# Performance work log

Measured on AMD Instinct MI355X. Metric: run time of the kernel, lower is better.

The kernel has to match this reference:

```python
import jax, jax.numpy as jnp
import numpy as np

T = 200000  # stack depth
V = 130     # vocab_size == input_dim
H = 512     # hid_dim
L = 2       # n_layers


def setup_inputs() -> dict:
    key = jax.random.key(0)
    ks = jax.random.split(key, 24)
    s = 0.05
    inp = {
        "input": jax.random.normal(ks[0], (1, 1, V), jnp.float32),
        "prev_Val": jax.random.normal(ks[1], (T, V), jnp.float32),
        "prev_stg": jax.random.uniform(ks[2], (T,), jnp.float32),
        "prev_read": jax.random.normal(ks[3], (V,), jnp.float32),
        "prev_h": jax.random.normal(ks[4], (L, 1, H), jnp.float32) * 0.1,
        "prev_c": jax.random.normal(ks[5], (L, 1, H), jnp.float32) * 0.1,
        # LSTM layer 0 (pytorch layout: W_ih (4H, in), W_hh (4H, H), gates i,f,g,o)
        "W_ih0": jax.random.normal(ks[6], (4 * H, V), jnp.float32) * s,
        "W_hh0": jax.random.normal(ks[7], (4 * H, H), jnp.float32) * s,
        "b_ih0": jax.random.normal(ks[8], (4 * H,), jnp.float32) * s,
        "b_hh0": jax.random.normal(ks[9], (4 * H,), jnp.float32) * s,
        # LSTM layer 1
        "W_ih1": jax.random.normal(ks[10], (4 * H, H), jnp.float32) * s,
        "W_hh1": jax.random.normal(ks[11], (4 * H, H), jnp.float32) * s,
        "b_ih1": jax.random.normal(ks[12], (4 * H,), jnp.float32) * s,
        "b_hh1": jax.random.normal(ks[13], (4 * H,), jnp.float32) * s,
        # gate heads (original inits these to zeros; random here to exercise math)
        "Wd": jax.random.normal(ks[14], (H,), jnp.float32) * s,
        "Bd": jax.random.normal(ks[15], (), jnp.float32) * s,
        "Wu": jax.random.normal(ks[16], (H,), jnp.float32) * s,
        "Bu": jax.random.normal(ks[17], (), jnp.float32) * s,
        "Wv": jax.random.normal(ks[18], (H, V), jnp.float32) * s,
        "Bv": jax.random.normal(ks[19], (V,), jnp.float32) * s,
        "Wo": jax.random.normal(ks[20], (H, H), jnp.float32) * s,
        "Bo": jax.random.normal(ks[21], (H,), jnp.float32) * s,
    }
    return inp


def _lstm_cell(x, h, c, Wih, Whh, bih, bhh):
    # x: (1, in), h/c: (1, H)
    g = x @ Wih.T + h @ Whh.T + bih + bhh  # (1, 4H)
    i, f, gg, o = jnp.split(g, 4, axis=-1)
    c2 = jax.nn.sigmoid(f) * c + jax.nn.sigmoid(i) * jnp.tanh(gg)
    h2 = jax.nn.sigmoid(o) * jnp.tanh(c2)
    return h2, c2


def reference(input, prev_Val, prev_stg, prev_read, prev_h, prev_c,
              W_ih0, W_hh0, b_ih0, b_hh0, W_ih1, W_hh1, b_ih1, b_hh1,
              Wd, Bd, Wu, Bu, Wv, Bv, Wo, Bo):
    x = (input + prev_read)[0]  # (1, V), seq_len == 1, batch == 1
    h1, c1 = _lstm_cell(x, prev_h[0], prev_c[0], W_ih0, W_hh0, b_ih0, b_hh0)
    h2, c2 = _lstm_cell(h1, prev_h[1], prev_c[1], W_ih1, W_hh1, b_ih1, b_hh1)
    output = h2  # (1, H)

    dt = jax.nn.sigmoid(output @ Wd + Bd)[0]      # scalar push strength
    ut = jax.nn.sigmoid(output @ Wu + Bu)[0]      # scalar pop strength
    vt = jnp.tanh(output @ Wv + Bv)               # (1, V) pushed value
    ot = jnp.tanh(output @ Wo + Bo)               # (1, H) controller output

    Val = jnp.concatenate([prev_Val, vt], axis=0)  # (T+1, V)

    # pop pass (top -> bottom): stg[i] = max(0, prev_stg[i] - max(0, ut)); ut -= stg[i]
    def pop_step(u, s):
        sn = jnp.maximum(0.0, s - jnp.maximum(0.0, u))
        return u - sn, sn
    _, stg_popped = jax.lax.scan(pop_step, ut, prev_stg, reverse=True)
    stg = jnp.concatenate([stg_popped, dt[None]])  # (T+1,)

    # read pass (top -> bottom): coef = min(stg[i], max(0, read)); read -= stg[i]
    def read_step(r, s):
        coef = jnp.minimum(s, jnp.maximum(0.0, r))
        return r - s, coef
    _, coefs = jax.lax.scan(read_step, jnp.asarray(1.0, stg.dtype), stg, reverse=True)
    rt = coefs @ Val  # (V,)

    h_new = jnp.stack([h1, h2])  # (L, 1, H)
    c_new = jnp.stack([c1, c2])
    return ot, Val, stg, rt, h_new, c_new
```

## Files before the change

kernel.cpp:

```cpp
#include <hip/hip_runtime.h>

#define T_DEPTH 200000
#define V_DIM   130
#define H_DIM   512

#define OT_OFF   0
#define VAL_OFF  512
#define STG_OFF  26000642
#define RT_OFF   26200643
#define HN_OFF   26200773
#define CN_OFF   26201797

#define WS_G0     0
#define WS_H1     2048
#define WS_C1     2560
#define WS_G1     3072
#define WS_H2     5120
#define WS_C2     5632
#define WS_VTACC  6144
#define WS_OTACC  6274
#define WS_DTUT   6786
#define WS_VT     6788
#define WS_TOTAL  6918

static __device__ __forceinline__ float sigmoidf(float x) {
    return 1.0f / (1.0f + expf(-x));
}

__global__ void k_bulk(const float4* __restrict__ val_in,
                       const float2* __restrict__ stg_in,
                       float* __restrict__ out) {
    const int NV4 = (T_DEPTH * V_DIM) / 4;
    const int NS2 = T_DEPTH / 2;
    const int NT  = NV4 + NS2;
    float4* __restrict__ val_out = reinterpret_cast<float4*>(out + VAL_OFF);
    float2* __restrict__ stg_out = reinterpret_cast<float2*>(out + STG_OFF);
    int stride = gridDim.x * blockDim.x;
    for (int u = blockIdx.x * blockDim.x + threadIdx.x; u < NT; u += stride) {
        if (u < NV4) {
            val_out[u] = val_in[u];
        } else {
            int s = u - NV4;
            stg_out[s] = stg_in[s];
        }
    }
}

__global__ void k_g0(const float* __restrict__ Wih, const float* __restrict__ Whh,
                     const float* __restrict__ bih, const float* __restrict__ bhh,
                     const float* __restrict__ inp, const float* __restrict__ prd,
                     const float* __restrict__ h0, float* __restrict__ g) {
    int wave = threadIdx.x >> 6, lane = threadIdx.x & 63;
    int row = blockIdx.x * 4 + wave;
    const float* wr = Wih + row * V_DIM;
    const float* wh = Whh + row * H_DIM;
    float p = 0.f;
    for (int c = lane; c < V_DIM; c += 64) p += wr[c] * (inp[c] + prd[c]);
    for (int k = lane; k < H_DIM; k += 64) p += wh[k] * h0[k];
    for (int off = 32; off; off >>= 1) p += __shfl_down(p, off, 64);
    if (lane == 0) g[row] = p + bih[row] + bhh[row];
}

__global__ void k_g1(const float* __restrict__ Wih, const float* __restrict__ Whh,
                     const float* __restrict__ bih, const float* __restrict__ bhh,
                     const float* __restrict__ h1, const float* __restrict__ hprev,
                     float* __restrict__ g) {
    int wave = threadIdx.x >> 6, lane = threadIdx.x & 63;
    int row = blockIdx.x * 4 + wave;
    const float* wr = Wih + row * H_DIM;
    const float* wh = Whh + row * H_DIM;
    float p = 0.f;
    for (int k = lane; k < H_DIM; k += 64) p += wr[k] * h1[k] + wh[k] * hprev[k];
    for (int off = 32; off; off >>= 1) p += __shfl_down(p, off, 64);
    if (lane == 0) g[row] = p + bih[row] + bhh[row];
}

__global__ void k_cell(const float* __restrict__ g, const float* __restrict__ cprev,
                       float* __restrict__ h, float* __restrict__ c,
                       float* __restrict__ h_out, float* __restrict__ c_out) {
    int j = threadIdx.x;
    float ig = sigmoidf(g[j]);
    float fg = sigmoidf(g[H_DIM + j]);
    float gg = tanhf(g[2 * H_DIM + j]);
    float og = sigmoidf(g[3 * H_DIM + j]);
    float cn = fg * cprev[j] + ig * gg;
    float hn = og * tanhf(cn);
    h[j] = hn; c[j] = cn;
    h_out[j] = hn;
    c_out[j] = cn;
}

__global__ void k_heads(const float* __restrict__ h2, const float* __restrict__ Wv,
                        const float* __restrict__ Wo, float* __restrict__ vt_acc,
                        float* __restrict__ ot_acc) {
    int t = threadIdx.x;
    int b = blockIdx.x;
    float a0 = 0.f, a1 = 0.f, av = 0.f;
    for (int kk = 0; kk < 16; ++kk) {
        int k = b * 16 + kk;
        float hv = h2[k];
        a0 += hv * Wo[k * H_DIM + t];
        a1 += hv * Wo[k * H_DIM + t + 256];
        if (t < V_DIM) av += hv * Wv[k * V_DIM + t];
    }
    atomicAdd(&ot_acc[t], a0);
    atomicAdd(&ot_acc[t + 256], a1);
    if (t < V_DIM) atomicAdd(&vt_acc[t], av);
}

__global__ void k_hfin(const float* __restrict__ h2,
                       const float* __restrict__ Wd, const float* __restrict__ Bd,
                       const float* __restrict__ Wu, const float* __restrict__ Bu,
                       const float* __restrict__ Bv, const float* __restrict__ Bo,
                       const float* __restrict__ vt_acc, const float* __restrict__ ot_acc,
                       float* __restrict__ dtut, float* __restrict__ vt,
                       float* __restrict__ out) {
    __shared__ float sd[H_DIM], su[H_DIM];
    int t = threadIdx.x;
    sd[t] = h2[t] * Wd[t];
    su[t] = h2[t] * Wu[t];
    __syncthreads();
    for (int s = 256; s; s >>= 1) {
        if (t < s) { sd[t] += sd[t + s]; su[t] += su[t + s]; }
        __syncthreads();
    }
    if (t == 0) {
        float dt = sigmoidf(sd[0] + Bd[0]);
        float ut = sigmoidf(su[0] + Bu[0]);
        dtut[0] = dt; dtut[1] = ut;
        out[STG_OFF + T_DEPTH] = dt;
    }
    float ot = tanhf(ot_acc[t] + Bo[t]);
    out[OT_OFF + t] = ot;
    if (t < V_DIM) {
        float v = tanhf(vt_acc[t] + Bv[t]);
        vt[t] = v;
        out[VAL_OFF + T_DEPTH * V_DIM + t] = v;
    }
}

__global__ void k_top(const float* __restrict__ prev_stg, const float* __restrict__ prev_val,
                      const float* __restrict__ dtut, const float* __restrict__ vt,
                      float* __restrict__ out) {
    int t = threadIdx.x;
    float dt = dtut[0];
    float u  = dtut[1];
    float r  = 1.0f;
    float acc = 0.f;
    {
        float coef = fminf(dt, fmaxf(0.f, r));
        if (t < V_DIM) acc += coef * vt[t];
        r -= dt;
    }
    for (int i = T_DEPTH - 1; i >= 0; --i) {
        bool pop_active = (u > 0.f);
        if (!pop_active && r <= 0.f) break;
        float s  = prev_stg[i];
        float sn = fmaxf(0.f, s - fmaxf(0.f, u));
        u -= sn;
        if (pop_active && t == 0) out[STG_OFF + i] = sn;
        float coef = fminf(sn, fmaxf(0.f, r));
        r -= sn;
        if (coef > 0.f && t < V_DIM) acc += coef * prev_val[i * V_DIM + t];
    }
    if (t < V_DIM) out[RT_OFF + t] = acc;
}

extern "C" void kernel_launch(void* const* d_in, const int* in_sizes, int n_in,
                              void* d_out, int out_size, void* d_ws, size_t ws_size,
                              hipStream_t stream) {
    (void)in_sizes; (void)n_in; (void)out_size; (void)ws_size;
    const float* input     = (const float*)d_in[0];
    const float* prev_Val  = (const float*)d_in[1];
    const float* prev_stg  = (const float*)d_in[2];
    const float* prev_read = (const float*)d_in[3];
    const float* prev_h    = (const float*)d_in[4];
    const float* prev_c    = (const float*)d_in[5];
    const float* W_ih0 = (const float*)d_in[6];
    const float* W_hh0 = (const float*)d_in[7];
    const float* b_ih0 = (const float*)d_in[8];
    const float* b_hh0 = (const float*)d_in[9];
    const float* W_ih1 = (const float*)d_in[10];
    const float* W_hh1 = (const float*)d_in[11];
    const float* b_ih1 = (const float*)d_in[12];
    const float* b_hh1 = (const float*)d_in[13];
    const float* Wd = (const float*)d_in[14];
    const float* Bd = (const float*)d_in[15];
    const float* Wu = (const float*)d_in[16];
    const float* Bu = (const float*)d_in[17];
    const float* Wv = (const float*)d_in[18];
    const float* Bv = (const float*)d_in[19];
    const float* Wo = (const float*)d_in[20];
    const float* Bo = (const float*)d_in[21];

    float* out = (float*)d_out;
    float* ws  = (float*)d_ws;

    hipMemsetAsync(d_ws, 0, WS_TOTAL * sizeof(float), stream);

    k_bulk<<<4096, 256, 0, stream>>>((const float4*)prev_Val, (const float2*)prev_stg, out);

    k_g0<<<512, 256, 0, stream>>>(W_ih0, W_hh0, b_ih0, b_hh0, input, prev_read,
                                  prev_h, ws + WS_G0);
    k_cell<<<1, 512, 0, stream>>>(ws + WS_G0, prev_c, ws + WS_H1, ws + WS_C1,
                                  out + HN_OFF, out + CN_OFF);
    k_g1<<<512, 256, 0, stream>>>(W_ih1, W_hh1, b_ih1, b_hh1, ws + WS_H1,
                                  prev_h + H_DIM, ws + WS_G1);
    k_cell<<<1, 512, 0, stream>>>(ws + WS_G1, prev_c + H_DIM, ws + WS_H2, ws + WS_C2,
                                  out + HN_OFF + H_DIM, out + CN_OFF + H_DIM);

    k_heads<<<32, 256, 0, stream>>>(ws + WS_H2, Wv, Wo, ws + WS_VTACC, ws + WS_OTACC);
    k_hfin<<<1, 512, 0, stream>>>(ws + WS_H2, Wd, Bd, Wu, Bu, Bv, Bo,
                                  ws + WS_VTACC, ws + WS_OTACC,
                                  ws + WS_DTUT, ws + WS_VT, out);

    k_top<<<1, 192, 0, stream>>>(prev_stg, prev_Val, ws + WS_DTUT, ws + WS_VT, out);
}
```

Before: 273.9 us.

## Fuse all stages into one persistent kernel with grid barriers and overlapped copy

Replaces the eight-kernel chain (bulk copy, two gate GEMVs, two cell kernels, heads, finalize, top scan) with one launch. Sixty-four chain blocks step through the LSTM and heads using atomic grid barriers, while 256 extra blocks copy prev_Val with nontemporal loads and stores concurrently. The heads are computed without atomics, and only the stg prefix below the last popped index is copied after the scan, since the scan already wrote the entries above it. This removes launch overhead and serialization between stages. It relies on all chain blocks being co-resident for the spin barriers, and the copy now competes with the critical chain for bandwidth.

```diff
diff --git a/kernel.cpp b/kernel.cpp
--- a/kernel.cpp
+++ b/kernel.cpp
@@ -11,159 +11,206 @@
 #define HN_OFF   26200773
 #define CN_OFF   26201797
 
-#define WS_G0     0
-#define WS_H1     2048
-#define WS_C1     2560
-#define WS_G1     3072
-#define WS_H2     5120
-#define WS_C2     5632
-#define WS_VTACC  6144
-#define WS_OTACC  6274
-#define WS_DTUT   6786
-#define WS_VT     6788
-#define WS_TOTAL  6918
+#define CHAIN_BLOCKS 64
+#define COPY_BLOCKS  256
+#define GRID_BLOCKS  (CHAIN_BLOCKS + COPY_BLOCKS)
+
+#define WS_ISTOP  16
+#define WS_G0     32
+#define WS_G1     2080
+#define WS_VT     4160
+#define WS_DTUT   4300
+
+typedef float fvec4 __attribute__((ext_vector_type(4)));
 
 static __device__ __forceinline__ float sigmoidf(float x) {
     return 1.0f / (1.0f + expf(-x));
 }
 
-__global__ void k_bulk(const float4* __restrict__ val_in,
-                       const float2* __restrict__ stg_in,
-                       float* __restrict__ out) {
-    const int NV4 = (T_DEPTH * V_DIM) / 4;
-    const int NS2 = T_DEPTH / 2;
-    const int NT  = NV4 + NS2;
-    float4* __restrict__ val_out = reinterpret_cast<float4*>(out + VAL_OFF);
-    float2* __restrict__ stg_out = reinterpret_cast<float2*>(out + STG_OFF);
-    int stride = gridDim.x * blockDim.x;
-    for (int u = blockIdx.x * blockDim.x + threadIdx.x; u < NT; u += stride) {
-        if (u < NV4) {
-            val_out[u] = val_in[u];
+static __device__ __forceinline__ void gbar(int* bar) {
+    __syncthreads();
+    if (threadIdx.x == 0) {
+        __hip_atomic_fetch_add(bar, 1, __ATOMIC_RELEASE, __HIP_MEMORY_SCOPE_AGENT);
+        while (__hip_atomic_load(bar, __ATOMIC_ACQUIRE, __HIP_MEMORY_SCOPE_AGENT)
+               < CHAIN_BLOCKS)
+            __builtin_amdgcn_s_sleep(8);
+    }
+    __syncthreads();
+}
+
+__global__ __launch_bounds__(256) void k_fused(
+        const float* __restrict__ input, const float* __restrict__ prev_Val,
+        const float* __restrict__ prev_stg, const float* __restrict__ prev_read,
+        const float* __restrict__ prev_h, const float* __restrict__ prev_c,
+        const float* __restrict__ W_ih0, const float* __restrict__ W_hh0,
+        const float* __restrict__ b_ih0, const float* __restrict__ b_hh0,
+        const float* __restrict__ W_ih1, const float* __restrict__ W_hh1,
+        const float* __restrict__ b_ih1, const float* __restrict__ b_hh1,
+        const float* __restrict__ Wd, const float* __restrict__ Bd,
+        const float* __restrict__ Wu, const float* __restrict__ Bu,
+        const float* __restrict__ Wv, const float* __restrict__ Bv,
+        const float* __restrict__ Wo, const float* __restrict__ Bo,
+        float* __restrict__ out, int* __restrict__ wsi, float* __restrict__ wsf) {
+
+    const int b = blockIdx.x;
+    const int t = threadIdx.x;
+
+    if (b >= CHAIN_BLOCKS) {
+        const int cb = b - CHAIN_BLOCKS;
+        const fvec4* __restrict__ vi = (const fvec4*)prev_Val;
+        fvec4* __restrict__ vo = (fvec4*)(out + VAL_OFF);
+        const int NV4 = (T_DEPTH * V_DIM) / 4;
+        for (int idx = cb * 256 + t; idx < NV4; idx += COPY_BLOCKS * 256) {
+            fvec4 v = __builtin_nontemporal_load(&vi[idx]);
+            __builtin_nontemporal_store(v, &vo[idx]);
+        }
+        return;
+    }
+
+    __shared__ float sh_h1[H_DIM];
+    __shared__ float sh_h2[H_DIM];
+    const int wave = t >> 6, lane = t & 63;
+
+    {
+        const float* h0 = prev_h;
+        for (int r = 0; r < 8; ++r) {
+            int row = (b * 4 + wave) + 256 * r;
+            const float* wr = W_ih0 + row * V_DIM;
+            const float* wh = W_hh0 + row * H_DIM;
+            float p = 0.f;
+            for (int c = lane; c < V_DIM; c += 64) p += wr[c] * (input[c] + prev_read[c]);
+            for (int k = lane; k < H_DIM; k += 64) p += wh[k] * h0[k];
+            for (int off = 32; off; off >>= 1) p += __shfl_down(p, off, 64);
+            if (lane == 0) wsf[WS_G0 + row] = p + b_ih0[row] + b_hh0[row];
+        }
+    }
+    gbar(&wsi[0]);
+
+    {
+        const float* g0 = wsf + WS_G0;
+        for (int r = 0; r < 2; ++r) {
+            int j = t + 256 * r;
+            float ig = sigmoidf(g0[j]);
+            float fg = sigmoidf(g0[H_DIM + j]);
+            float gg = tanhf(g0[2 * H_DIM + j]);
+            float og = sigmoidf(g0[3 * H_DIM + j]);
+            float cn = fg * prev_c[j] + ig * gg;
+            float hn = og * tanhf(cn);
+            sh_h1[j] = hn;
+            if (b == 0) { out[HN_OFF + j] = hn; out[CN_OFF + j] = cn; }
+        }
+        __syncthreads();
+        const float* h1p = prev_h + H_DIM;
+        for (int r = 0; r < 8; ++r) {
+            int row = (b * 4 + wave) + 256 * r;
+            const float* wr = W_ih1 + row * H_DIM;
+            const float* wh = W_hh1 + row * H_DIM;
+            float p = 0.f;
+            for (int k = lane; k < H_DIM; k += 64) p += wr[k] * sh_h1[k] + wh[k] * h1p[k];
+            for (int off = 32; off; off >>= 1) p += __shfl_down(p, off, 64);
+            if (lane == 0) wsf[WS_G1 + row] = p + b_ih1[row] + b_hh1[row];
+        }
+    }
+    gbar(&wsi[1]);
+
+    if (b < 4) {
+        const float* g1 = wsf + WS_G1;
+        const float* c1p = prev_c + H_DIM;
+        for (int r = 0; r < 2; ++r) {
+            int j = t + 256 * r;
+            float ig = sigmoidf(g1[j]);
+            float fg = sigmoidf(g1[H_DIM + j]);
+            float gg = tanhf(g1[2 * H_DIM + j]);
+            float og = sigmoidf(g1[3 * H_DIM + j]);
+            float cn = fg * c1p[j] + ig * gg;
+            float hn = og * tanhf(cn);
+            sh_h2[j] = hn;
+            if (b == 0) { out[HN_OFF + H_DIM + j] = hn; out[CN_OFF + H_DIM + j] = cn; }
+        }
+        __syncthreads();
+
+        if (b <= 1) {
+            int j = b * 256 + t;
+            float a0 = 0.f, a1 = 0.f, a2 = 0.f, a3 = 0.f;
+            for (int k = 0; k < H_DIM; k += 4) {
+                a0 += sh_h2[k]     * Wo[(k)     * H_DIM + j];
+                a1 += sh_h2[k + 1] * Wo[(k + 1) * H_DIM + j];
+                a2 += sh_h2[k + 2] * Wo[(k + 2) * H_DIM + j];
+                a3 += sh_h2[k + 3] * Wo[(k + 3) * H_DIM + j];
+            }
+            out[OT_OFF + j] = tanhf(a0 + a1 + a2 + a3 + Bo[j]);
+        } else if (b == 2) {
+            if (t < V_DIM) {
+                float a0 = 0.f, a1 = 0.f, a2 = 0.f, a3 = 0.f;
+                for (int k = 0; k < H_DIM; k += 4) {
+                    a0 += sh_h2[k]     * Wv[(k)     * V_DIM + t];
+                    a1 += sh_h2[k + 1] * Wv[(k + 1) * V_DIM + t];
+                    a2 += sh_h2[k + 2] * Wv[(k + 2) * V_DIM + t];
+                    a3 += sh_h2[k + 3] * Wv[(k + 3) * V_DIM + t];
+                }
+                float v = tanhf(a0 + a1 + a2 + a3 + Bv[t]);
+                wsf[WS_VT + t] = v;
+                out[VAL_OFF + (size_t)T_DEPTH * V_DIM + t] = v;
+            }
         } else {
-            int s = u - NV4;
-            stg_out[s] = stg_in[s];
-        }
-    }
-}
-
-__global__ void k_g0(const float* __restrict__ Wih, const float* __restrict__ Whh,
-                     const float* __restrict__ bih, const float* __restrict__ bhh,
-                     const float* __restrict__ inp, const float* __restrict__ prd,
-                     const float* __restrict__ h0, float* __restrict__ g) {
-    int wave = threadIdx.x >> 6, lane = threadIdx.x & 63;
-    int row = blockIdx.x * 4 + wave;
-    const float* wr = Wih + row * V_DIM;
-    const float* wh = Whh + row * H_DIM;
-    float p = 0.f;
-    for (int c = lane; c < V_DIM; c += 64) p += wr[c] * (inp[c] + prd[c]);
-    for (int k = lane; k < H_DIM; k += 64) p += wh[k] * h0[k];
-    for (int off = 32; off; off >>= 1) p += __shfl_down(p, off, 64);
-    if (lane == 0) g[row] = p + bih[row] + bhh[row];
-}
-
-__global__ void k_g1(const float* __restrict__ Wih, const float* __restrict__ Whh,
-                     const float* __restrict__ bih, const float* __restrict__ bhh,
-                     const float* __restrict__ h1, const float* __restrict__ hprev,
-                     float* __restrict__ g) {
-    int wave = threadIdx.x >> 6, lane = threadIdx.x & 63;
-    int row = blockIdx.x * 4 + wave;
-    const float* wr = Wih + row * H_DIM;
-    const float* wh = Whh + row * H_DIM;
-    float p = 0.f;
-    for (int k = lane; k < H_DIM; k += 64) p += wr[k] * h1[k] + wh[k] * hprev[k];
-    for (int off = 32; off; off >>= 1) p += __shfl_down(p, off, 64);
-    if (lane == 0) g[row] = p + bih[row] + bhh[row];
-}
-
-__global__ void k_cell(const float* __restrict__ g, const float* __restrict__ cprev,
-                       float* __restrict__ h, float* __restrict__ c,
-                       float* __restrict__ h_out, float* __restrict__ c_out) {
-    int j = threadIdx.x;
-    float ig = sigmoidf(g[j]);
-    float fg = sigmoidf(g[H_DIM + j]);
-    float gg = tanhf(g[2 * H_DIM + j]);
-    float og = sigmoidf(g[3 * H_DIM + j]);
-    float cn = fg * cprev[j] + ig * gg;
-    float hn = og * tanhf(cn);
-    h[j] = hn; c[j] = cn;
-    h_out[j] = hn;
-    c_out[j] = cn;
-}
-
-__global__ void k_heads(const float* __restrict__ h2, const float* __restrict__ Wv,
-                        const float* __restrict__ Wo, float* __restrict__ vt_acc,
-                        float* __restrict__ ot_acc) {
-    int t = threadIdx.x;
-    int b = blockIdx.x;
-    float a0 = 0.f, a1 = 0.f, av = 0.f;
-    for (int kk = 0; kk < 16; ++kk) {
-        int k = b * 16 + kk;
-        float hv = h2[k];
-        a0 += hv * Wo[k * H_DIM + t];
-        a1 += hv * Wo[k * H_DIM + t + 256];
-        if (t < V_DIM) av += hv * Wv[k * V_DIM + t];
-    }
-    atomicAdd(&ot_acc[t], a0);
-    atomicAdd(&ot_acc[t + 256], a1);
-    if (t < V_DIM) atomicAdd(&vt_acc[t], av);
-}
-
-__global__ void k_hfin(const float* __restrict__ h2,
-                       const float* __restrict__ Wd, const float* __restrict__ Bd,
-                       const float* __restrict__ Wu, const float* __restrict__ Bu,
-                       const float* __restrict__ Bv, const float* __restrict__ Bo,
-                       const float* __restrict__ vt_acc, const float* __restrict__ ot_acc,
-                       float* __restrict__ dtut, float* __restrict__ vt,
-                       float* __restrict__ out) {
-    __shared__ float sd[H_DIM], su[H_DIM];
-    int t = threadIdx.x;
-    sd[t] = h2[t] * Wd[t];
-    su[t] = h2[t] * Wu[t];
-    __syncthreads();
-    for (int s = 256; s; s >>= 1) {
-        if (t < s) { sd[t] += sd[t + s]; su[t] += su[t + s]; }
-        __syncthreads();
-    }
-    if (t == 0) {
-        float dt = sigmoidf(sd[0] + Bd[0]);
-        float ut = sigmoidf(su[0] + Bu[0]);
-        dtut[0] = dt; dtut[1] = ut;
-        out[STG_OFF + T_DEPTH] = dt;
-    }
-    float ot = tanhf(ot_acc[t] + Bo[t]);
-    out[OT_OFF + t] = ot;
-    if (t < V_DIM) {
-        float v = tanhf(vt_acc[t] + Bv[t]);
-        vt[t] = v;
-        out[VAL_OFF + T_DEPTH * V_DIM + t] = v;
-    }
-}
-
-__global__ void k_top(const float* __restrict__ prev_stg, const float* __restrict__ prev_val,
-                      const float* __restrict__ dtut, const float* __restrict__ vt,
-                      float* __restrict__ out) {
-    int t = threadIdx.x;
-    float dt = dtut[0];
-    float u  = dtut[1];
-    float r  = 1.0f;
-    float acc = 0.f;
+            if (wave < 2) {
+                const float* w = (wave == 0) ? Wd : Wu;
+                float p = 0.f;
+                for (int k = lane; k < H_DIM; k += 64) p += sh_h2[k] * w[k];
+                for (int off = 32; off; off >>= 1) p += __shfl_down(p, off, 64);
+                if (lane == 0) {
+                    if (wave == 0) {
+                        float dt = sigmoidf(p + Bd[0]);
+                        wsf[WS_DTUT + 0] = dt;
+                        out[STG_OFF + T_DEPTH] = dt;
+                    } else {
+                        wsf[WS_DTUT + 1] = sigmoidf(p + Bu[0]);
+                    }
+                }
+            }
+        }
+    }
+    gbar(&wsi[2]);
+
+    if (b == 0) {
+        float dt = wsf[WS_DTUT + 0];
+        float u  = wsf[WS_DTUT + 1];
+        float r  = 1.0f;
+        float acc = 0.f;
+        {
+            float coef = fminf(dt, fmaxf(0.f, r));
+            if (t < V_DIM) acc += coef * wsf[WS_VT + t];
+            r -= dt;
+        }
+        int last = T_DEPTH;
+        for (int i = T_DEPTH - 1; i >= 0; --i) {
+            bool pa = (u > 0.f);
+            if (!pa && r <= 0.f) break;
+            float s  = prev_stg[i];
+            float sn = fmaxf(0.f, s - fmaxf(0.f, u));
+            u -= sn;
+            if (pa) { if (t == 0) out[STG_OFF + i] = sn; last = i; }
+            float coef = fminf(sn, fmaxf(0.f, r));
+            r -= sn;
+            if (coef > 0.f && t < V_DIM) acc += coef * prev_Val[(size_t)i * V_DIM + t];
+        }
+        if (t < V_DIM) out[RT_OFF + t] = acc;
+        if (t == 0) __hip_atomic_store(&wsi[WS_ISTOP], last, __ATOMIC_RELEASE,
+                                       __HIP_MEMORY_SCOPE_AGENT);
+    }
+    gbar(&wsi[3]);
+
     {
-        float coef = fminf(dt, fmaxf(0.f, r));
-        if (t < V_DIM) acc += coef * vt[t];
-        r -= dt;
-    }
-    for (int i = T_DEPTH - 1; i >= 0; --i) {
-        bool pop_active = (u > 0.f);
-        if (!pop_active && r <= 0.f) break;
-        float s  = prev_stg[i];
-        float sn = fmaxf(0.f, s - fmaxf(0.f, u));
-        u -= sn;
-        if (pop_active && t == 0) out[STG_OFF + i] = sn;
-        float coef = fminf(sn, fmaxf(0.f, r));
-        r -= sn;
-        if (coef > 0.f && t < V_DIM) acc += coef * prev_val[i * V_DIM + t];
-    }
-    if (t < V_DIM) out[RT_OFF + t] = acc;
+        int istop = __hip_atomic_load(&wsi[WS_ISTOP], __ATOMIC_ACQUIRE,
+                                      __HIP_MEMORY_SCOPE_AGENT);
+        const float2* __restrict__ si = (const float2*)prev_stg;
+        float2* __restrict__ so = (float2*)(out + STG_OFF);
+        int np = istop >> 1;
+        for (int idx = b * 256 + t; idx < np; idx += CHAIN_BLOCKS * 256)
+            so[idx] = si[idx];
+        if (b == 0 && t == 0 && (istop & 1))
+            out[STG_OFF + istop - 1] = prev_stg[istop - 1];
+    }
 }
 
 extern "C" void kernel_launch(void* const* d_in, const int* in_sizes, int n_in,
@@ -194,25 +241,13 @@
     const float* Bo = (const float*)d_in[21];
 
     float* out = (float*)d_out;
-    float* ws  = (float*)d_ws;
-
-    hipMemsetAsync(d_ws, 0, WS_TOTAL * sizeof(float), stream);
-
-    k_bulk<<<4096, 256, 0, stream>>>((const float4*)prev_Val, (const float2*)prev_stg, out);
-
-    k_g0<<<512, 256, 0, stream>>>(W_ih0, W_hh0, b_ih0, b_hh0, input, prev_read,
-                                  prev_h, ws + WS_G0);
-    k_cell<<<1, 512, 0, stream>>>(ws + WS_G0, prev_c, ws + WS_H1, ws + WS_C1,
-                                  out + HN_OFF, out + CN_OFF);
-    k_g1<<<512, 256, 0, stream>>>(W_ih1, W_hh1, b_ih1, b_hh1, ws + WS_H1,
-                                  prev_h + H_DIM, ws + WS_G1);
-    k_cell<<<1, 512, 0, stream>>>(ws + WS_G1, prev_c + H_DIM, ws + WS_H2, ws + WS_C2,
-                                  out + HN_OFF + H_DIM, out + CN_OFF + H_DIM);
-
-    k_heads<<<32, 256, 0, stream>>>(ws + WS_H2, Wv, Wo, ws + WS_VTACC, ws + WS_OTACC);
-    k_hfin<<<1, 512, 0, stream>>>(ws + WS_H2, Wd, Bd, Wu, Bu, Bv, Bo,
-                                  ws + WS_VTACC, ws + WS_OTACC,
-                                  ws + WS_DTUT, ws + WS_VT, out);
-
-    k_top<<<1, 192, 0, stream>>>(prev_stg, prev_Val, ws + WS_DTUT, ws + WS_VT, out);
-}
+    int*   wsi = (int*)d_ws;
+    float* wsf = (float*)d_ws;
+
+    (void)hipMemsetAsync(d_ws, 0, 256, stream);
+
+    k_fused<<<GRID_BLOCKS, 256, 0, stream>>>(
+        input, prev_Val, prev_stg, prev_read, prev_h, prev_c,
+        W_ih0, W_hh0, b_ih0, b_hh0, W_ih1, W_hh1, b_ih1, b_hh1,
+        Wd, Bd, Wu, Bu, Wv, Bv, Wo, Bo, out, wsi, wsf);
+}
```

Result: slower. 319.7 us (+16.7%).
